# Kernel tuning notes

Hardware: AMD Instinct MI355X
Metric: run time of the kernel (lower is better)

The kernel has to match this reference:

```python
import jax, jax.numpy as jnp
import numpy as np

N = 100000      # hits
P = 512         # particle ids (0 = noise, skipped)
D = 8           # condensation-space dim
Q_MIN = 0.01
REPULSION_SCALING = 10.0


def setup_inputs() -> dict:
    key = jax.random.key(0)
    k1, k2, k3, k4, k5 = jax.random.split(key, 5)
    w = jax.random.normal(k1, (N,), dtype=jnp.float32)
    # beta in (0, 0.95) so arctanh stays well-conditioned
    beta = jax.random.uniform(k2, (N,), dtype=jnp.float32) * 0.95
    x = jax.random.normal(k3, (N, D), dtype=jnp.float32)
    y = jax.random.normal(k4, (N,), dtype=jnp.float32)
    particle_id = jax.random.randint(k5, (N,), 0, P)
    return {"w": w, "beta": beta, "x": x, "y": y, "particle_id": particle_id}


def _safe_sqrt(s):
    # sqrt with zero (sub)gradient at 0, matching torch.norm's behavior at 0
    pos = s > 0
    return jnp.where(pos, jnp.sqrt(jnp.where(pos, s, 1.0)), 0.0)


def _condensation_loss(beta, x, particle_id):
    n = beta.shape[0]
    q = jnp.arctanh(beta) ** 2 + Q_MIN                     # [N]
    # per-particle condensation point: hit with max q (torch.argmax -> first)
    q_max = jax.ops.segment_max(q, particle_id, num_segments=P)          # [P]
    counts = jax.ops.segment_sum(jnp.ones_like(q), particle_id, num_segments=P)
    is_max = q == q_max[particle_id]
    cand = jnp.where(is_max, jnp.arange(n), n)
    alpha_idx = jnp.clip(jax.ops.segment_min(cand, particle_id, num_segments=P), 0, n - 1)
    valid = (counts > 0) & (jnp.arange(P) != 0)            # skip noise pid 0 and absent pids
    q_alpha = jnp.where(valid, q_max, 0.0)                 # [P], sanitized (-inf for empty segs)
    x_alpha = x[alpha_idx]                                  # [P, D]
    # squared distances [N, P] via GEMM (avoids [N, P, D] intermediate)
    sq = (jnp.sum(x * x, axis=1, keepdims=True)
          - 2.0 * (x @ x_alpha.T)
          + jnp.sum(x_alpha * x_alpha, axis=1)[None, :])
    sq = jnp.maximum(sq, 0.0)
    dist = _safe_sqrt(sq)
    va = sq * q_alpha[None, :]                              # attractive potential
    vr = jnp.maximum(1.0 - dist, 0.0) * q_alpha[None, :]    # repulsive hinge
    M = (particle_id[:, None] == jnp.arange(P)[None, :]).astype(x.dtype)  # [N, P]
    per_p = jnp.mean(q[:, None] * (M * va + REPULSION_SCALING * (1.0 - M) * vr), axis=0)  # [P]
    return jnp.sum(jnp.where(valid, per_p, 0.0))


def reference(w, beta, x, y, particle_id):
    return _condensation_loss(beta, x, particle_id)
```

## Files before the change

kernel.cpp:

```cpp
#include <hip/hip_runtime.h>

#define P_IDS 512
#define DIM 8
#define QMIN 0.01f
#define REP 10.0f
#define CHUNK 64
#define NCHUNK (P_IDS / CHUNK)
#define HPT 4
#define HB (256 * HPT)

typedef unsigned long long ull;

__launch_bounds__(256)
__global__ void stageA_kernel(const float* __restrict__ beta,
                              const int* __restrict__ pid,
                              float* __restrict__ q_out,
                              ull* __restrict__ tables,
                              int n) {
    __shared__ ull s_keys[P_IDS];
    s_keys[threadIdx.x] = 0ULL;
    s_keys[threadIdx.x + 256] = 0ULL;
    __syncthreads();
    int i = blockIdx.x * 256 + threadIdx.x;
    if (i < n) {
        float b = beta[i];
        float at = 0.5f * logf((1.0f + b) / (1.0f - b));
        float qv = fmaf(at, at, QMIN);
        q_out[i] = qv;
        ull key = ((ull)__float_as_uint(qv) << 32) |
                  (ull)(unsigned int)(~(unsigned int)i);
        atomicMax(&s_keys[pid[i]], key);
    }
    __syncthreads();
    ull* dst = tables + (size_t)blockIdx.x * P_IDS;
    dst[threadIdx.x] = s_keys[threadIdx.x];
    dst[threadIdx.x + 256] = s_keys[threadIdx.x + 256];
}

__launch_bounds__(64)
__global__ void stageB_kernel(const ull* __restrict__ tables, int ntab,
                              const float* __restrict__ x,
                              float2* __restrict__ meta,
                              float* __restrict__ x_alpha,
                              float* __restrict__ out) {
    int p = blockIdx.x;
    ull k = 0ULL;
    for (int t = threadIdx.x; t < ntab; t += 64) {
        ull v = tables[(size_t)t * P_IDS + p];
        k = (v > k) ? v : k;
    }
#pragma unroll
    for (int off = 32; off > 0; off >>= 1) {
        ull o = __shfl_down(k, off, 64);
        k = (o > k) ? o : k;
    }
    if (threadIdx.x == 0) {
        bool valid = (k != 0ULL) && (p != 0);
        float qa = valid ? __uint_as_float((unsigned int)(k >> 32)) : 0.0f;
        int idx = valid ? (int)(~(unsigned int)(k & 0xFFFFFFFFull)) : 0;
        float4 a = ((const float4*)x)[idx * 2];
        float4 b = ((const float4*)x)[idx * 2 + 1];
        float xa2 = a.x * a.x;
        xa2 = fmaf(a.y, a.y, xa2); xa2 = fmaf(a.z, a.z, xa2); xa2 = fmaf(a.w, a.w, xa2);
        xa2 = fmaf(b.x, b.x, xa2); xa2 = fmaf(b.y, b.y, xa2); xa2 = fmaf(b.z, b.z, xa2);
        xa2 = fmaf(b.w, b.w, xa2);
        ((float4*)x_alpha)[p * 2] = a;
        ((float4*)x_alpha)[p * 2 + 1] = b;
        meta[p] = make_float2(qa, xa2);
        if (p == 0) out[0] = 0.0f;
    }
}

__launch_bounds__(256)
__global__ void loss_kernel(const float* __restrict__ x,
                            const float* __restrict__ q,
                            const int* __restrict__ pid,
                            const float2* __restrict__ meta,
                            const float* __restrict__ x_alpha,
                            float* __restrict__ out,
                            int n) {
    __shared__ float  s_xa[CHUNK * DIM];
    __shared__ float2 s_meta[CHUNK];
    int chunk = blockIdx.x & (NCHUNK - 1);
    int hb    = blockIdx.x / NCHUNK;
    int p0    = chunk * CHUNK;
    if (threadIdx.x < CHUNK * DIM / 4)
        ((float4*)s_xa)[threadIdx.x] =
            ((const float4*)(x_alpha + p0 * DIM))[threadIdx.x];
    if (threadIdx.x < CHUNK) s_meta[threadIdx.x] = meta[p0 + threadIdx.x];
    __syncthreads();

    float xi[HPT][DIM], xi2[HPT], qi[HPT], acc[HPT];
    int   myj[HPT];
    int base = hb * HB + threadIdx.x;
#pragma unroll
    for (int h = 0; h < HPT; ++h) {
        int i = base + h * 256;
        bool act = i < n;
        int ii = act ? i : 0;
        float4 v0 = ((const float4*)x)[ii * 2];
        float4 v1 = ((const float4*)x)[ii * 2 + 1];
        xi[h][0] = v0.x; xi[h][1] = v0.y; xi[h][2] = v0.z; xi[h][3] = v0.w;
        xi[h][4] = v1.x; xi[h][5] = v1.y; xi[h][6] = v1.z; xi[h][7] = v1.w;
        float s = 0.0f;
#pragma unroll
        for (int d = 0; d < DIM; ++d) s = fmaf(xi[h][d], xi[h][d], s);
        xi2[h] = s;
        qi[h]  = act ? q[ii] : 0.0f;
        myj[h] = act ? (pid[ii] - p0) : -1;
        acc[h] = 0.0f;
    }

    for (int j = 0; j < CHUNK; ++j) {
        float2 m  = s_meta[j];
        float4 a0 = ((const float4*)s_xa)[j * 2];
        float4 a1 = ((const float4*)s_xa)[j * 2 + 1];
        float sq[HPT];
#pragma unroll
        for (int h = 0; h < HPT; ++h) {
            float dot = xi[h][0] * a0.x;
            dot = fmaf(xi[h][1], a0.y, dot); dot = fmaf(xi[h][2], a0.z, dot);
            dot = fmaf(xi[h][3], a0.w, dot); dot = fmaf(xi[h][4], a1.x, dot);
            dot = fmaf(xi[h][5], a1.y, dot); dot = fmaf(xi[h][6], a1.z, dot);
            dot = fmaf(xi[h][7], a1.w, dot);
            sq[h] = fmaxf(fmaf(-2.0f, dot, xi2[h] + m.y), 0.0f);
        }
        float mn = fminf(fminf(sq[0], sq[1]), fminf(sq[2], sq[3]));
        if (__any(mn < 1.0f)) {
#pragma unroll
            for (int h = 0; h < HPT; ++h) {
                float vr = fmaxf(1.0f - __builtin_amdgcn_sqrtf(sq[h]), 0.0f);
                acc[h] = fmaf(vr, m.x, acc[h]);
            }
        }
    }

    float partial = 0.0f;
#pragma unroll
    for (int h = 0; h < HPT; ++h) {
        float t = REP * acc[h];
        int j = myj[h];
        if (j >= 0 && j < CHUNK) {
            float2 m = s_meta[j];
            float dot = xi[h][0] * s_xa[j * DIM + 0];
#pragma unroll
            for (int d = 1; d < DIM; ++d) dot = fmaf(xi[h][d], s_xa[j * DIM + d], dot);
            float sq = fmaxf(fmaf(-2.0f, dot, xi2[h] + m.y), 0.0f);
            float vr = fmaxf(1.0f - __builtin_amdgcn_sqrtf(sq), 0.0f);
            t += m.x * (sq - REP * vr);
        }
        partial = fmaf(qi[h], t, partial);
    }

#pragma unroll
    for (int off = 32; off > 0; off >>= 1)
        partial += __shfl_down(partial, off, 64);
    __shared__ float s_red[4];
    if ((threadIdx.x & 63) == 0) s_red[threadIdx.x >> 6] = partial;
    __syncthreads();
    if (threadIdx.x == 0)
        atomicAdd(out, (s_red[0] + s_red[1] + s_red[2] + s_red[3]) / (float)n);
}

extern "C" void kernel_launch(void* const* d_in, const int* in_sizes, int n_in,
                              void* d_out, int out_size, void* d_ws, size_t ws_size,
                              hipStream_t stream) {
    int n = in_sizes[0];
    const float* beta = (const float*)d_in[1];
    const float* x    = (const float*)d_in[2];
    const int*   pid  = (const int*)d_in[4];
    float* out = (float*)d_out;

    int a_blocks = (n + 255) / 256;
    char* ws = (char*)d_ws;
    size_t tab_bytes = (size_t)a_blocks * P_IDS * sizeof(ull);
    tab_bytes = (tab_bytes + 255) & ~(size_t)255;
    size_t q_bytes = (((size_t)n * 4) + 255) & ~(size_t)255;
    ull*    tables  = (ull*)ws;
    float*  q       = (float*)(ws + tab_bytes);
    float2* meta    = (float2*)(ws + tab_bytes + q_bytes);
    float*  x_alpha = (float*)(ws + tab_bytes + q_bytes + P_IDS * sizeof(float2));

    stageA_kernel<<<a_blocks, 256, 0, stream>>>(beta, pid, q, tables, n);
    stageB_kernel<<<P_IDS, 64, 0, stream>>>(tables, a_blocks, x, meta, x_alpha, out);
    int hit_blocks = (n + HB - 1) / HB;
    loss_kernel<<<hit_blocks * NCHUNK, 256, 0, stream>>>(x, q, pid, meta, x_alpha, out, n);
}
```

Before: 97.37 us.

## Compute hit-to-condensation-point distances with bf16x3-split MFMA instead of scalar FMAs

The loss kernel now computes the N x P dot products with matrix-core MFMA 16x16x32 bf16 instructions. Each fp32 vector is split into high and low bf16 parts and packed so a single 32-wide K dimension holds the hi*hi, lo*hi and hi*lo terms, keeping roughly fp32 accuracy. Each block handles 64 hits against all 512 particles, with the B operand staged in LDS and the attractive term computed separately per hit. This removes most scalar FMA work from the hot loop, but it adds bf16 split-precision error and a different block decomposition.

```diff
diff --git a/kernel.cpp b/kernel.cpp
--- a/kernel.cpp
+++ b/kernel.cpp
@@ -4,12 +4,32 @@
 #define DIM 8
 #define QMIN 0.01f
 #define REP 10.0f
-#define CHUNK 64
-#define NCHUNK (P_IDS / CHUNK)
-#define HPT 4
-#define HB (256 * HPT)
 
 typedef unsigned long long ull;
+typedef float f32x4 __attribute__((ext_vector_type(4)));
+typedef short s16x8 __attribute__((ext_vector_type(8)));
+
+__device__ __forceinline__ unsigned int bf16_rne(float f) {
+    unsigned int u = __float_as_uint(f);
+    return (u + 0x7FFFu + ((u >> 16) & 1u)) >> 16;
+}
+__device__ __forceinline__ float bf16_to_f32(unsigned int h) {
+    return __uint_as_float(h << 16);
+}
+__device__ __forceinline__ void split_pack(const float* v, uint4& hiw, uint4& low) {
+    unsigned int hb[8], lb[8];
+#pragma unroll
+    for (int d = 0; d < 8; ++d) {
+        unsigned int h = bf16_rne(v[d]);
+        float rem = v[d] - bf16_to_f32(h);
+        hb[d] = h;
+        lb[d] = bf16_rne(rem);
+    }
+    hiw = make_uint4(hb[0] | (hb[1] << 16), hb[2] | (hb[3] << 16),
+                     hb[4] | (hb[5] << 16), hb[6] | (hb[7] << 16));
+    low = make_uint4(lb[0] | (lb[1] << 16), lb[2] | (lb[3] << 16),
+                     lb[4] | (lb[5] << 16), lb[6] | (lb[7] << 16));
+}
 
 __launch_bounds__(256)
 __global__ void stageA_kernel(const float* __restrict__ beta,
@@ -42,6 +62,7 @@
                               const float* __restrict__ x,
                               float2* __restrict__ meta,
                               float* __restrict__ x_alpha,
+                              uint4* __restrict__ gB,
                               float* __restrict__ out) {
     int p = blockIdx.x;
     ull k = 0ULL;
@@ -67,6 +88,10 @@
         ((float4*)x_alpha)[p * 2] = a;
         ((float4*)x_alpha)[p * 2 + 1] = b;
         meta[p] = make_float2(qa, xa2);
+        float xv[8] = {a.x, a.y, a.z, a.w, b.x, b.y, b.z, b.w};
+        uint4 hiw, low; split_pack(xv, hiw, low);
+        gB[p] = hiw;
+        gB[P_IDS + p] = low;
         if (p == 0) out[0] = 0.0f;
     }
 }
@@ -77,88 +102,98 @@
                             const int* __restrict__ pid,
                             const float2* __restrict__ meta,
                             const float* __restrict__ x_alpha,
-                            float* __restrict__ out,
-                            int n) {
-    __shared__ float  s_xa[CHUNK * DIM];
-    __shared__ float2 s_meta[CHUNK];
-    int chunk = blockIdx.x & (NCHUNK - 1);
-    int hb    = blockIdx.x / NCHUNK;
-    int p0    = chunk * CHUNK;
-    if (threadIdx.x < CHUNK * DIM / 4)
-        ((float4*)s_xa)[threadIdx.x] =
-            ((const float4*)(x_alpha + p0 * DIM))[threadIdx.x];
-    if (threadIdx.x < CHUNK) s_meta[threadIdx.x] = meta[p0 + threadIdx.x];
-    __syncthreads();
-
-    float xi[HPT][DIM], xi2[HPT], qi[HPT], acc[HPT];
-    int   myj[HPT];
-    int base = hb * HB + threadIdx.x;
-#pragma unroll
-    for (int h = 0; h < HPT; ++h) {
-        int i = base + h * 256;
+                            const uint4* __restrict__ gB,
+                            float* __restrict__ out, int n) {
+    __shared__ uint4  s_B[2 * P_IDS];
+    __shared__ float2 s_meta[P_IDS];
+    __shared__ uint4  s_A[128];
+    __shared__ __align__(16) float s_xi2[64];
+    __shared__ __align__(16) float s_qi[64];
+    __shared__ __align__(16) int   s_pid[64];
+
+    int tid = threadIdx.x;
+    float partial = 0.0f;
+
+    if (tid < 64) {
+        int i = blockIdx.x * 64 + tid;
         bool act = i < n;
         int ii = act ? i : 0;
         float4 v0 = ((const float4*)x)[ii * 2];
         float4 v1 = ((const float4*)x)[ii * 2 + 1];
-        xi[h][0] = v0.x; xi[h][1] = v0.y; xi[h][2] = v0.z; xi[h][3] = v0.w;
-        xi[h][4] = v1.x; xi[h][5] = v1.y; xi[h][6] = v1.z; xi[h][7] = v1.w;
+        float xv[8] = {v0.x, v0.y, v0.z, v0.w, v1.x, v1.y, v1.z, v1.w};
         float s = 0.0f;
 #pragma unroll
-        for (int d = 0; d < DIM; ++d) s = fmaf(xi[h][d], xi[h][d], s);
-        xi2[h] = s;
-        qi[h]  = act ? q[ii] : 0.0f;
-        myj[h] = act ? (pid[ii] - p0) : -1;
-        acc[h] = 0.0f;
-    }
-
-    for (int j = 0; j < CHUNK; ++j) {
-        float2 m  = s_meta[j];
-        float4 a0 = ((const float4*)s_xa)[j * 2];
-        float4 a1 = ((const float4*)s_xa)[j * 2 + 1];
-        float sq[HPT];
-#pragma unroll
-        for (int h = 0; h < HPT; ++h) {
-            float dot = xi[h][0] * a0.x;
-            dot = fmaf(xi[h][1], a0.y, dot); dot = fmaf(xi[h][2], a0.z, dot);
-            dot = fmaf(xi[h][3], a0.w, dot); dot = fmaf(xi[h][4], a1.x, dot);
-            dot = fmaf(xi[h][5], a1.y, dot); dot = fmaf(xi[h][6], a1.z, dot);
-            dot = fmaf(xi[h][7], a1.w, dot);
-            sq[h] = fmaxf(fmaf(-2.0f, dot, xi2[h] + m.y), 0.0f);
-        }
-        float mn = fminf(fminf(sq[0], sq[1]), fminf(sq[2], sq[3]));
+        for (int d = 0; d < 8; ++d) s = fmaf(xv[d], xv[d], s);
+        float qi = act ? q[ii] : 0.0f;
+        int   pd = act ? pid[ii] : 0;
+        s_xi2[tid] = act ? s : 0.0f;
+        s_qi[tid]  = qi;
+        s_pid[tid] = pd;
+        float m2[8];
+#pragma unroll
+        for (int d = 0; d < 8; ++d) m2[d] = act ? (-2.0f * xv[d]) : 0.0f;
+        uint4 hiw, low; split_pack(m2, hiw, low);
+        s_A[tid] = hiw; s_A[64 + tid] = low;
+        float2 mm = meta[pd];
+        float4 a0 = ((const float4*)x_alpha)[pd * 2];
+        float4 a1 = ((const float4*)x_alpha)[pd * 2 + 1];
+        float dot = xv[0] * a0.x;
+        dot = fmaf(xv[1], a0.y, dot); dot = fmaf(xv[2], a0.z, dot);
+        dot = fmaf(xv[3], a0.w, dot); dot = fmaf(xv[4], a1.x, dot);
+        dot = fmaf(xv[5], a1.y, dot); dot = fmaf(xv[6], a1.z, dot);
+        dot = fmaf(xv[7], a1.w, dot);
+        float sqe = fmaxf(fmaf(-2.0f, dot, s + mm.y), 0.0f);
+        partial = qi * mm.x * sqe;
+    }
+    for (int k = tid; k < 2 * P_IDS; k += 256) s_B[k] = gB[k];
+    for (int k = tid; k < P_IDS; k += 256) s_meta[k] = meta[k];
+    __syncthreads();
+
+    int lane = tid & 63;
+    int wid  = tid >> 6;
+    int grp  = lane >> 4;
+    int col  = lane & 15;
+
+    s16x8 av = *reinterpret_cast<const s16x8*>(
+        &s_A[((grp & 1) << 6) + wid * 16 + col]);
+    int rbase = wid * 16 + (grp << 2);
+    f32x4 xi2r = *reinterpret_cast<const f32x4*>(&s_xi2[rbase]);
+    f32x4 qir  = *reinterpret_cast<const f32x4*>(&s_qi[rbase]);
+    int4  pidr = *reinterpret_cast<const int4*>(&s_pid[rbase]);
+
+    const uint4* bptr = &s_B[((grp >= 2) ? P_IDS : 0) + col];
+    f32x4 rp = {0.0f, 0.0f, 0.0f, 0.0f};
+
+#pragma unroll
+    for (int jt = 0; jt < P_IDS / 16; ++jt) {
+        s16x8 bv = *reinterpret_cast<const s16x8*>(&bptr[jt * 16]);
+        float2 mm = s_meta[jt * 16 + col];
+        f32x4 c;
+        c[0] = xi2r[0] + mm.y; c[1] = xi2r[1] + mm.y;
+        c[2] = xi2r[2] + mm.y; c[3] = xi2r[3] + mm.y;
+        c = __builtin_amdgcn_mfma_f32_16x16x32_bf16(av, bv, c, 0, 0, 0);
+        float mn = fminf(fminf(c[0], c[1]), fminf(c[2], c[3]));
         if (__any(mn < 1.0f)) {
-#pragma unroll
-            for (int h = 0; h < HPT; ++h) {
-                float vr = fmaxf(1.0f - __builtin_amdgcn_sqrtf(sq[h]), 0.0f);
-                acc[h] = fmaf(vr, m.x, acc[h]);
+            int p = jt * 16 + col;
+#pragma unroll
+            for (int r = 0; r < 4; ++r) {
+                float sq = fmaxf(c[r], 0.0f);
+                float vr = fmaxf(1.0f - __builtin_amdgcn_sqrtf(sq), 0.0f);
+                float w  = (pidr[r] == p) ? 0.0f : mm.x;
+                rp[r] = fmaf(vr, w, rp[r]);
             }
         }
     }
-
-    float partial = 0.0f;
-#pragma unroll
-    for (int h = 0; h < HPT; ++h) {
-        float t = REP * acc[h];
-        int j = myj[h];
-        if (j >= 0 && j < CHUNK) {
-            float2 m = s_meta[j];
-            float dot = xi[h][0] * s_xa[j * DIM + 0];
-#pragma unroll
-            for (int d = 1; d < DIM; ++d) dot = fmaf(xi[h][d], s_xa[j * DIM + d], dot);
-            float sq = fmaxf(fmaf(-2.0f, dot, xi2[h] + m.y), 0.0f);
-            float vr = fmaxf(1.0f - __builtin_amdgcn_sqrtf(sq), 0.0f);
-            t += m.x * (sq - REP * vr);
-        }
-        partial = fmaf(qi[h], t, partial);
-    }
+    partial += REP * (qir[0] * rp[0] + qir[1] * rp[1] +
+                      qir[2] * rp[2] + qir[3] * rp[3]);
 
 #pragma unroll
     for (int off = 32; off > 0; off >>= 1)
         partial += __shfl_down(partial, off, 64);
     __shared__ float s_red[4];
-    if ((threadIdx.x & 63) == 0) s_red[threadIdx.x >> 6] = partial;
-    __syncthreads();
-    if (threadIdx.x == 0)
+    if ((tid & 63) == 0) s_red[tid >> 6] = partial;
+    __syncthreads();
+    if (tid == 0)
         atomicAdd(out, (s_red[0] + s_red[1] + s_red[2] + s_red[3]) / (float)n);
 }
 
@@ -177,12 +212,15 @@
     tab_bytes = (tab_bytes + 255) & ~(size_t)255;
     size_t q_bytes = (((size_t)n * 4) + 255) & ~(size_t)255;
     ull*    tables  = (ull*)ws;
-    float*  q       = (float*)(ws + tab_bytes);
-    float2* meta    = (float2*)(ws + tab_bytes + q_bytes);
-    float*  x_alpha = (float*)(ws + tab_bytes + q_bytes + P_IDS * sizeof(float2));
-
-    stageA_kernel<<<a_blocks, 256, 0, stream>>>(beta, pid, q, tables, n);
-    stageB_kernel<<<P_IDS, 64, 0, stream>>>(tables, a_blocks, x, meta, x_alpha, out);
-    int hit_blocks = (n + HB - 1) / HB;
-    loss_kernel<<<hit_blocks * NCHUNK, 256, 0, stream>>>(x, q, pid, meta, x_alpha, out, n);
-}
+    float*  qbuf    = (float*)(ws + tab_bytes);
+    char*   p0      = ws + tab_bytes + q_bytes;
+    float2* meta    = (float2*)p0;
+    float*  x_alpha = (float*)(p0 + P_IDS * sizeof(float2));
+    uint4*  gB      = (uint4*)(p0 + P_IDS * sizeof(float2)
+                                  + P_IDS * DIM * sizeof(float));
+
+    stageA_kernel<<<a_blocks, 256, 0, stream>>>(beta, pid, qbuf, tables, n);
+    stageB_kernel<<<P_IDS, 64, 0, stream>>>(tables, a_blocks, x, meta, x_alpha, gB, out);
+    int loss_blocks = (n + 63) / 64;
+    loss_kernel<<<loss_blocks, 256, 0, stream>>>(x, qbuf, pid, meta, x_alpha, gB, out, n);
+}
```

After: 102.5 us. 5.2% more time.
